# Kernel tuning notes

Measured on AMD Instinct MI355X. Metric: run time of the kernel, lower is better.

Reference implementation:

```python
import jax, jax.numpy as jnp
import numpy as np

D_MODEL = 1024
H = 16
D_K = D_MODEL // H
WINDOW = 256
NEG = -1.0e9


def setup_inputs() -> dict:
    key = jax.random.key(0)
    ks = jax.random.split(key, 12)
    B, S = 1, 4096
    scale = 1.0 / np.sqrt(D_MODEL)
    inp = {
        'q': jax.random.normal(ks[0], (B, S, D_MODEL), dtype=jnp.float32),
        'k': jax.random.normal(ks[1], (B, S, D_MODEL), dtype=jnp.float32),
        'v': jax.random.normal(ks[2], (B, S, D_MODEL), dtype=jnp.float32),
        'w_q': jax.random.normal(ks[3], (D_MODEL, D_MODEL), dtype=jnp.float32) * scale,
        'b_q': jnp.zeros((D_MODEL,), dtype=jnp.float32),
        'w_k': jax.random.normal(ks[4], (D_MODEL, D_MODEL), dtype=jnp.float32) * scale,
        'b_k': jnp.zeros((D_MODEL,), dtype=jnp.float32),
        'w_v': jax.random.normal(ks[5], (D_MODEL, D_MODEL), dtype=jnp.float32) * scale,
        'b_v': jnp.zeros((D_MODEL,), dtype=jnp.float32),
        'w_o': jax.random.normal(ks[6], (D_MODEL, D_MODEL), dtype=jnp.float32) * scale,
        'b_o': jnp.zeros((D_MODEL,), dtype=jnp.float32),
    }
    return inp


def _local_mask(seq_len: int, window_size: int) -> jnp.ndarray:
    left = (window_size - 1) // 2
    right = window_size - 1 - left
    row = jnp.arange(seq_len)[:, None]
    col = jnp.arange(seq_len)[None, :]
    return (col >= row - left) & (col <= row + right)  # [S, S] bool


def reference(q, k, v, w_q, b_q, w_k, b_k, w_v, b_v, w_o, b_o):
    B, Sq, _ = q.shape
    Sk = k.shape[1]
    # projections (torch Linear: x @ W.T + b) -> [B, h, S, d_k]
    query = (q @ w_q.T + b_q).reshape(B, Sq, H, D_K).transpose(0, 2, 1, 3)
    key = (k @ w_k.T + b_k).reshape(B, Sk, H, D_K).transpose(0, 2, 1, 3)
    value = (v @ w_v.T + b_v).reshape(B, Sk, H, D_K).transpose(0, 2, 1, 3)

    scores = jnp.einsum('bhqd,bhkd->bhqk', query, key) / jnp.sqrt(
        jnp.asarray(D_K, dtype=query.dtype))
    if Sq == Sk:
        mask = _local_mask(Sq, WINDOW)  # [S, S]
        scores = jnp.where(mask[None, None], scores, jnp.asarray(NEG, scores.dtype))
    attn = jax.nn.softmax(scores, axis=-1)
    x = jnp.einsum('bhqk,bhkd->bhqd', attn, value)
    x = x.transpose(0, 2, 1, 3).reshape(B, Sq, D_MODEL)
    return x @ w_o.T + b_o
```

## Files before the change

### kernel.cpp

```cpp
#include <hip/hip_runtime.h>

#define SEQ 4096
#define DM 1024
#define NH 16
#define DK 64

typedef _Float16 half8 __attribute__((ext_vector_type(8)));
typedef _Float16 half4v __attribute__((ext_vector_type(4)));
typedef float f32x4 __attribute__((ext_vector_type(4)));

#define MFMA16(a, b, c) __builtin_amdgcn_mfma_f32_16x16x32_f16((a), (b), (c), 0, 0, 0)
#define GLOAD_LDS(g, l)                                                                  \
    __builtin_amdgcn_global_load_lds((const __attribute__((address_space(1))) void*)(g), \
                                     (__attribute__((address_space(3))) void*)(l), 16, 0, 0)

__global__ void cvt_all(const float* __restrict__ q, const float* __restrict__ k,
                        const float* __restrict__ v, const float* __restrict__ wq,
                        const float* __restrict__ wk, const float* __restrict__ wv,
                        const float* __restrict__ wo, _Float16* __restrict__ qh,
                        _Float16* __restrict__ kh, _Float16* __restrict__ vh,
                        _Float16* __restrict__ wqh, _Float16* __restrict__ wkh,
                        _Float16* __restrict__ wvh, _Float16* __restrict__ woh) {
    int z = blockIdx.y;
    const float* src;
    _Float16* dst;
    int n;
    switch (z) {
    case 0: src = q;  dst = qh;  n = SEQ * DM; break;
    case 1: src = k;  dst = kh;  n = SEQ * DM; break;
    case 2: src = v;  dst = vh;  n = SEQ * DM; break;
    case 3: src = wq; dst = wqh; n = DM * DM;  break;
    case 4: src = wk; dst = wkh; n = DM * DM;  break;
    case 5: src = wv; dst = wvh; n = DM * DM;  break;
    default: src = wo; dst = woh; n = DM * DM; break;
    }
    int idx = (blockIdx.x * 256 + threadIdx.x) * 4;
    if (idx >= n) return;
    float4 f = *(const float4*)(src + idx);
    half4v h;
    h[0] = (_Float16)f.x; h[1] = (_Float16)f.y; h[2] = (_Float16)f.z; h[3] = (_Float16)f.w;
    *(half4v*)(dst + idx) = h;
}

template <int MT>
__device__ __forceinline__ void gemm_bk64(const _Float16* __restrict__ A,
                                          const _Float16* __restrict__ B, int m0, int n0,
                                          _Float16* As, _Float16* Bs, f32x4 (*acc)[4]) {
    constexpr int MI = MT / 32;
    constexpr int ACH = MT / 64;
    const int tid = threadIdx.x;
    const int wave = tid >> 6, lane = tid & 63;
    const int quad = lane >> 4, l16 = lane & 15;
    const int wr = (wave >> 1) * (MT / 2);
    const int wc = (wave & 1) * 64;
    const int srow = tid >> 2, scol = (tid & 3) * 8;

    for (int k0 = 0; k0 < DM; k0 += 64) {
#pragma unroll
        for (int p = 0; p < 2; ++p) {
            int kc = k0 + p * 32 + scol;
#pragma unroll
            for (int j = 0; j < ACH; ++j)
                GLOAD_LDS(A + (size_t)(m0 + j * 64 + srow) * DM + kc,
                          As + p * (MT * 32) + j * 2048 + tid * 8);
#pragma unroll
            for (int j = 0; j < 2; ++j)
                GLOAD_LDS(B + (size_t)(n0 + j * 64 + srow) * DM + kc,
                          Bs + p * 4096 + j * 2048 + tid * 8);
        }
        __syncthreads();
#pragma unroll
        for (int p = 0; p < 2; ++p) {
            half8 af[MI], bf[4];
#pragma unroll
            for (int mi = 0; mi < MI; ++mi)
                af[mi] = *(const half8*)&As[p * (MT * 32) + (wr + mi * 16 + l16) * 32 + quad * 8];
#pragma unroll
            for (int ni = 0; ni < 4; ++ni)
                bf[ni] = *(const half8*)&Bs[p * 4096 + (wc + ni * 16 + l16) * 32 + quad * 8];
#pragma unroll
            for (int mi = 0; mi < MI; ++mi)
#pragma unroll
                for (int ni = 0; ni < 4; ++ni)
                    acc[mi][ni] = MFMA16(af[mi], bf[ni], acc[mi][ni]);
        }
        __syncthreads();
    }
}

__global__ void __launch_bounds__(256, 3) gemm_qkv(
    const _Float16* __restrict__ qh, const _Float16* __restrict__ kh,
    const _Float16* __restrict__ vh, const _Float16* __restrict__ wqh,
    const _Float16* __restrict__ wkh, const _Float16* __restrict__ wvh,
    const float* __restrict__ bq, const float* __restrict__ bk, const float* __restrict__ bv,
    _Float16* __restrict__ Qo, _Float16* __restrict__ Ko, _Float16* __restrict__ Vt) {
    __shared__ _Float16 As[2 * 128 * 32];
    __shared__ _Float16 Bs[2 * 128 * 32];
    int z = blockIdx.z;
    const _Float16 *A, *B;
    const float* bias;
    float scale;
    if (z == 0) { A = qh; B = wqh; bias = bq; scale = 0.125f; }
    else if (z == 1) { A = kh; B = wkh; bias = bk; scale = 1.0f; }
    else { A = vh; B = wvh; bias = bv; scale = 1.0f; }

    int m0 = blockIdx.x * 128;
    int n0 = blockIdx.y * 128;
    f32x4 acc[4][4] = {};
    gemm_bk64<128>(A, B, m0, n0, As, Bs, acc);

    const int tid = threadIdx.x;
    const int wave = tid >> 6, lane = tid & 63;
    const int quad = lane >> 4, l16 = lane & 15;
    const int wr = (wave >> 1) * 64;
    const int wc = (wave & 1) * 64;
    float bs[4];
#pragma unroll
    for (int ni = 0; ni < 4; ++ni) bs[ni] = bias[n0 + wc + ni * 16 + l16];

    if (z < 2) {
        _Float16* C = (z == 0) ? Qo : Ko;
#pragma unroll
        for (int mi = 0; mi < 4; ++mi)
#pragma unroll
            for (int ni = 0; ni < 4; ++ni) {
                int m = m0 + wr + mi * 16 + quad * 4;
                int n = n0 + wc + ni * 16 + l16;
#pragma unroll
                for (int r = 0; r < 4; ++r)
                    C[(size_t)(m + r) * DM + n] = (_Float16)((acc[mi][ni][r] + bs[ni]) * scale);
            }
    } else {
#pragma unroll
        for (int mi = 0; mi < 4; ++mi)
#pragma unroll
            for (int ni = 0; ni < 4; ++ni) {
                int m = m0 + wr + mi * 16 + quad * 4;
                int n = n0 + wc + ni * 16 + l16;
                half4v p;
#pragma unroll
                for (int r = 0; r < 4; ++r) p[r] = (_Float16)(acc[mi][ni][r] + bs[ni]);
                *(half4v*)(Vt + (size_t)n * SEQ + m) = p;
            }
    }
}

__global__ void __launch_bounds__(256, 3) gemm_out(const _Float16* __restrict__ Xh,
                                                   const _Float16* __restrict__ woh,
                                                   const float* __restrict__ bo,
                                                   float* __restrict__ out) {
    __shared__ _Float16 As[2 * 64 * 32];
    __shared__ _Float16 Bs[2 * 128 * 32];
    int m0 = blockIdx.x * 64;
    int n0 = blockIdx.y * 128;
    f32x4 acc[2][4] = {};
    gemm_bk64<64>(Xh, woh, m0, n0, As, Bs, acc);

    const int tid = threadIdx.x;
    const int wave = tid >> 6, lane = tid & 63;
    const int quad = lane >> 4, l16 = lane & 15;
    const int wr = (wave >> 1) * 32;
    const int wc = (wave & 1) * 64;
#pragma unroll
    for (int mi = 0; mi < 2; ++mi)
#pragma unroll
        for (int ni = 0; ni < 4; ++ni) {
            int m = m0 + wr + mi * 16 + quad * 4;
            int n = n0 + wc + ni * 16 + l16;
            float b = bo[n];
#pragma unroll
            for (int r = 0; r < 4; ++r) out[(size_t)(m + r) * DM + n] = acc[mi][ni][r] + b;
        }
}

__global__ void attn_kernel(const _Float16* __restrict__ Q, const _Float16* __restrict__ K,
                            const _Float16* __restrict__ Vt, _Float16* __restrict__ X) {
    __shared__ _Float16 Pl[4][16][32];
    int tid = threadIdx.x;
    int wave = tid >> 6, lane = tid & 63;
    int quad = lane >> 4, l16 = lane & 15;
    int h = blockIdx.y;
    int bx = ((blockIdx.x & 7) << 3) + (blockIdx.x >> 3);
    int q0 = bx * 64 + wave * 16;

    const _Float16* Qp = Q + (size_t)(q0 + l16) * DM + h * DK + quad * 8;
    half8 aq0 = *(const half8*)(Qp);
    half8 aq1 = *(const half8*)(Qp + 32);

    float rowM[4], rowL[4];
    f32x4 o[4] = {};
#pragma unroll
    for (int r = 0; r < 4; ++r) { rowM[r] = -__builtin_inff(); rowL[r] = 0.f; }

    int kstart = (q0 > 127) ? ((q0 - 127) & ~31) : 0;
    int kend = q0 + 143;
    if (kend > SEQ - 1) kend = SEQ - 1;

    for (int kt = kstart; kt <= kend; kt += 32) {
        f32x4 s[2];
#pragma unroll
        for (int cf = 0; cf < 2; ++cf) {
            int krow = kt + cf * 16 + l16;
            const _Float16* Kp = K + (size_t)krow * DM + h * DK + quad * 8;
            half8 b0 = *(const half8*)(Kp);
            half8 b1 = *(const half8*)(Kp + 32);
            f32x4 z = {};
            z = MFMA16(aq0, b0, z);
            z = MFMA16(aq1, b1, z);
            s[cf] = z;
        }
        float mnew[4], alpha[4];
#pragma unroll
        for (int r = 0; r < 4; ++r) {
            int row = q0 + quad * 4 + r;
#pragma unroll
            for (int cf = 0; cf < 2; ++cf) {
                int key = kt + cf * 16 + l16;
                bool valid = (key >= row - 127) && (key <= row + 128);
                if (!valid) s[cf][r] = -1e30f;
            }
            float t = fmaxf(s[0][r], s[1][r]);
#pragma unroll
            for (int off = 1; off < 16; off <<= 1) t = fmaxf(t, __shfl_xor(t, off));
            mnew[r] = fmaxf(rowM[r], t);
            alpha[r] = __expf(rowM[r] - mnew[r]);
            float p0 = __expf(s[0][r] - mnew[r]);
            float p1 = __expf(s[1][r] - mnew[r]);
            Pl[wave][quad * 4 + r][l16] = (_Float16)p0;
            Pl[wave][quad * 4 + r][l16 + 16] = (_Float16)p1;
            float rs = p0 + p1;
#pragma unroll
            for (int off = 1; off < 16; off <<= 1) rs += __shfl_xor(rs, off);
            rowL[r] = rowL[r] * alpha[r] + rs;
            rowM[r] = mnew[r];
        }
#pragma unroll
        for (int ni = 0; ni < 4; ++ni)
#pragma unroll
            for (int r = 0; r < 4; ++r) o[ni][r] *= alpha[r];
        half8 ap = *(const half8*)&Pl[wave][l16][quad * 8];
#pragma unroll
        for (int ni = 0; ni < 4; ++ni) {
            const _Float16* Vp = Vt + (size_t)(h * DK + ni * 16 + l16) * SEQ + kt + quad * 8;
            half8 bv = *(const half8*)(Vp);
            o[ni] = MFMA16(ap, bv, o[ni]);
        }
    }

    float rinv[4];
#pragma unroll
    for (int r = 0; r < 4; ++r) rinv[r] = 1.0f / rowL[r];
#pragma unroll
    for (int ni = 0; ni < 4; ++ni) {
        int n = h * DK + ni * 16 + l16;
#pragma unroll
        for (int r = 0; r < 4; ++r) {
            int m = q0 + quad * 4 + r;
            X[(size_t)m * DM + n] = (_Float16)(o[ni][r] * rinv[r]);
        }
    }
}

extern "C" void kernel_launch(void* const* d_in, const int* in_sizes, int n_in, void* d_out,
                              int out_size, void* d_ws, size_t ws_size, hipStream_t stream) {
    const float* q  = (const float*)d_in[0];
    const float* k  = (const float*)d_in[1];
    const float* v  = (const float*)d_in[2];
    const float* wq = (const float*)d_in[3];
    const float* bq = (const float*)d_in[4];
    const float* wk = (const float*)d_in[5];
    const float* bk = (const float*)d_in[6];
    const float* wv = (const float*)d_in[7];
    const float* bv = (const float*)d_in[8];
    const float* wo = (const float*)d_in[9];
    const float* bo = (const float*)d_in[10];

    const size_t SZ_T = (size_t)SEQ * DM * sizeof(_Float16);
    const size_t SZ_W = (size_t)DM * DM * sizeof(_Float16);
    char* p = (char*)d_ws;
    _Float16* qh  = (_Float16*)(p);
    _Float16* kh  = (_Float16*)(p + SZ_T);
    _Float16* vh  = (_Float16*)(p + 2 * SZ_T);
    _Float16* wqh = (_Float16*)(p + 3 * SZ_T);
    _Float16* wkh = (_Float16*)(p + 3 * SZ_T + SZ_W);
    _Float16* wvh = (_Float16*)(p + 3 * SZ_T + 2 * SZ_W);
    _Float16* woh = (_Float16*)(p + 3 * SZ_T + 3 * SZ_W);
    _Float16* Qo  = (_Float16*)(p + 3 * SZ_T + 4 * SZ_W);
    _Float16* Ko  = (_Float16*)(p + 4 * SZ_T + 4 * SZ_W);
    _Float16* Vt  = (_Float16*)(p + 5 * SZ_T + 4 * SZ_W);
    _Float16* Xh  = qh;

    cvt_all<<<dim3(4096, 7), 256, 0, stream>>>(q, k, v, wq, wk, wv, wo, qh, kh, vh, wqh, wkh,
                                               wvh, woh);
    gemm_qkv<<<dim3(32, 8, 3), 256, 0, stream>>>(qh, kh, vh, wqh, wkh, wvh, bq, bk, bv, Qo, Ko,
                                                 Vt);
    attn_kernel<<<dim3(SEQ / 64, NH), 256, 0, stream>>>(Qo, Ko, Vt, Xh);
    gemm_out<<<dim3(64, 8), 256, 0, stream>>>(Xh, woh, bo, (float*)d_out);
}
```

Baseline: 213.6 us.

## Software-pipeline attention K loads, MFMA row sums, and widen conversion kernel

The attention loop becomes a fixed 10-tile fully unrolled loop with K fragments double-buffered in registers and V loads issued before the score MFMAs, so memory latency overlaps compute. The row-sum shuffle reduction is replaced by an MFMA of the probability tile against a ones vector, and launch bounds are added. The conversion kernel now processes 8 elements per thread with half the grid. Edge tiles are clamped and masked, which adds some redundant work for sequence-boundary blocks.

```diff
diff --git a/kernel.cpp b/kernel.cpp
--- a/kernel.cpp
+++ b/kernel.cpp
@@ -34,12 +34,14 @@
     case 5: src = wv; dst = wvh; n = DM * DM;  break;
     default: src = wo; dst = woh; n = DM * DM; break;
     }
-    int idx = (blockIdx.x * 256 + threadIdx.x) * 4;
+    int idx = (blockIdx.x * 256 + threadIdx.x) * 8;
     if (idx >= n) return;
-    float4 f = *(const float4*)(src + idx);
-    half4v h;
-    h[0] = (_Float16)f.x; h[1] = (_Float16)f.y; h[2] = (_Float16)f.z; h[3] = (_Float16)f.w;
-    *(half4v*)(dst + idx) = h;
+    float4 f0 = *(const float4*)(src + idx);
+    float4 f1 = *(const float4*)(src + idx + 4);
+    half8 h;
+    h[0] = (_Float16)f0.x; h[1] = (_Float16)f0.y; h[2] = (_Float16)f0.z; h[3] = (_Float16)f0.w;
+    h[4] = (_Float16)f1.x; h[5] = (_Float16)f1.y; h[6] = (_Float16)f1.z; h[7] = (_Float16)f1.w;
+    *(half8*)(dst + idx) = h;
 }
 
 template <int MT>
@@ -173,78 +175,95 @@
         }
 }
 
-__global__ void attn_kernel(const _Float16* __restrict__ Q, const _Float16* __restrict__ K,
-                            const _Float16* __restrict__ Vt, _Float16* __restrict__ X) {
+__global__ void __launch_bounds__(256, 4) attn_kernel(const _Float16* __restrict__ Q,
+                                                      const _Float16* __restrict__ K,
+                                                      const _Float16* __restrict__ Vt,
+                                                      _Float16* __restrict__ X) {
     __shared__ _Float16 Pl[4][16][32];
-    int tid = threadIdx.x;
-    int wave = tid >> 6, lane = tid & 63;
-    int quad = lane >> 4, l16 = lane & 15;
-    int h = blockIdx.y;
-    int bx = ((blockIdx.x & 7) << 3) + (blockIdx.x >> 3);
-    int q0 = bx * 64 + wave * 16;
+    const int tid = threadIdx.x;
+    const int wave = tid >> 6, lane = tid & 63;
+    const int quad = lane >> 4, l16 = lane & 15;
+    const int h = blockIdx.y;
+    const int bx = ((blockIdx.x & 7) << 3) + (blockIdx.x >> 3);
+    const int q0 = bx * 64 + wave * 16;
 
     const _Float16* Qp = Q + (size_t)(q0 + l16) * DM + h * DK + quad * 8;
-    half8 aq0 = *(const half8*)(Qp);
-    half8 aq1 = *(const half8*)(Qp + 32);
+    const half8 aq0 = *(const half8*)(Qp);
+    const half8 aq1 = *(const half8*)(Qp + 32);
+    const half8 ones = {(_Float16)1, (_Float16)1, (_Float16)1, (_Float16)1,
+                        (_Float16)1, (_Float16)1, (_Float16)1, (_Float16)1};
 
     float rowM[4], rowL[4];
     f32x4 o[4] = {};
 #pragma unroll
     for (int r = 0; r < 4; ++r) { rowM[r] = -__builtin_inff(); rowL[r] = 0.f; }
 
-    int kstart = (q0 > 127) ? ((q0 - 127) & ~31) : 0;
-    int kend = q0 + 143;
-    if (kend > SEQ - 1) kend = SEQ - 1;
-
-    for (int kt = kstart; kt <= kend; kt += 32) {
-        f32x4 s[2];
-#pragma unroll
-        for (int cf = 0; cf < 2; ++cf) {
-            int krow = kt + cf * 16 + l16;
-            const _Float16* Kp = K + (size_t)krow * DM + h * DK + quad * 8;
-            half8 b0 = *(const half8*)(Kp);
-            half8 b1 = *(const half8*)(Kp + 32);
-            f32x4 z = {};
-            z = MFMA16(aq0, b0, z);
-            z = MFMA16(aq1, b1, z);
-            s[cf] = z;
-        }
-        float mnew[4], alpha[4];
+    const int kstart = (q0 > 127) ? ((q0 - 127) & ~31) : 0;
+
+    auto loadK = [&](int kt, half8* kb) {
+        int kr0 = kt + l16;       kr0 = kr0 < SEQ ? kr0 : SEQ - 1;
+        int kr1 = kt + 16 + l16;  kr1 = kr1 < SEQ ? kr1 : SEQ - 1;
+        const _Float16* p0 = K + (size_t)kr0 * DM + h * DK + quad * 8;
+        const _Float16* p1 = K + (size_t)kr1 * DM + h * DK + quad * 8;
+        kb[0] = *(const half8*)p0;
+        kb[1] = *(const half8*)(p0 + 32);
+        kb[2] = *(const half8*)p1;
+        kb[3] = *(const half8*)(p1 + 32);
+    };
+
+    auto body = [&](int kt, const half8* kb) {
+        int vcol = kt + quad * 8;
+        int vc = vcol < SEQ ? vcol : 0;
+        half8 vv[4];
+#pragma unroll
+        for (int ni = 0; ni < 4; ++ni)
+            vv[ni] = *(const half8*)(Vt + (size_t)(h * DK + ni * 16 + l16) * SEQ + vc);
+
+        f32x4 s0 = {}, s1 = {};
+        s0 = MFMA16(aq0, kb[0], s0);
+        s0 = MFMA16(aq1, kb[1], s0);
+        s1 = MFMA16(aq0, kb[2], s1);
+        s1 = MFMA16(aq1, kb[3], s1);
+
+        const int key0 = kt + l16, key1 = kt + 16 + l16;
+        float alpha[4];
 #pragma unroll
         for (int r = 0; r < 4; ++r) {
             int row = q0 + quad * 4 + r;
-#pragma unroll
-            for (int cf = 0; cf < 2; ++cf) {
-                int key = kt + cf * 16 + l16;
-                bool valid = (key >= row - 127) && (key <= row + 128);
-                if (!valid) s[cf][r] = -1e30f;
-            }
-            float t = fmaxf(s[0][r], s[1][r]);
-#pragma unroll
-            for (int off = 1; off < 16; off <<= 1) t = fmaxf(t, __shfl_xor(t, off));
-            mnew[r] = fmaxf(rowM[r], t);
-            alpha[r] = __expf(rowM[r] - mnew[r]);
-            float p0 = __expf(s[0][r] - mnew[r]);
-            float p1 = __expf(s[1][r] - mnew[r]);
-            Pl[wave][quad * 4 + r][l16] = (_Float16)p0;
-            Pl[wave][quad * 4 + r][l16 + 16] = (_Float16)p1;
-            float rs = p0 + p1;
-#pragma unroll
-            for (int off = 1; off < 16; off <<= 1) rs += __shfl_xor(rs, off);
-            rowL[r] = rowL[r] * alpha[r] + rs;
-            rowM[r] = mnew[r];
-        }
-#pragma unroll
-        for (int ni = 0; ni < 4; ++ni)
+            float x0 = (key0 >= row - 127 && key0 <= row + 128 && key0 < SEQ) ? s0[r] : -1e30f;
+            float x1 = (key1 >= row - 127 && key1 <= row + 128 && key1 < SEQ) ? s1[r] : -1e30f;
+            float m = fmaxf(x0, x1);
+#pragma unroll
+            for (int off = 1; off < 16; off <<= 1) m = fmaxf(m, __shfl_xor(m, off));
+            float mnew = fmaxf(rowM[r], m);
+            alpha[r] = __expf(rowM[r] - mnew);
+            float p0f = __expf(x0 - mnew);
+            float p1f = __expf(x1 - mnew);
+            Pl[wave][quad * 4 + r][l16] = (_Float16)p0f;
+            Pl[wave][quad * 4 + r][l16 + 16] = (_Float16)p1f;
+            rowM[r] = mnew;
+        }
+        half8 ap = *(const half8*)&Pl[wave][l16][quad * 8];
+        f32x4 ts = {};
+        ts = MFMA16(ap, ones, ts);
+#pragma unroll
+        for (int r = 0; r < 4; ++r) rowL[r] = rowL[r] * alpha[r] + ts[r];
+#pragma unroll
+        for (int ni = 0; ni < 4; ++ni) {
 #pragma unroll
             for (int r = 0; r < 4; ++r) o[ni][r] *= alpha[r];
-        half8 ap = *(const half8*)&Pl[wave][l16][quad * 8];
-#pragma unroll
-        for (int ni = 0; ni < 4; ++ni) {
-            const _Float16* Vp = Vt + (size_t)(h * DK + ni * 16 + l16) * SEQ + kt + quad * 8;
-            half8 bv = *(const half8*)(Vp);
-            o[ni] = MFMA16(ap, bv, o[ni]);
-        }
+            o[ni] = MFMA16(ap, vv[ni], o[ni]);
+        }
+    };
+
+    half8 kbA[4], kbB[4];
+    loadK(kstart, kbA);
+#pragma unroll
+    for (int tt = 0; tt < 5; ++tt) {
+        loadK(kstart + (tt * 2 + 1) * 32, kbB);
+        body(kstart + tt * 2 * 32, kbA);
+        if (tt < 4) loadK(kstart + (tt * 2 + 2) * 32, kbA);
+        body(kstart + (tt * 2 + 1) * 32, kbB);
     }
 
     float rinv[4];
@@ -290,7 +309,7 @@
     _Float16* Vt  = (_Float16*)(p + 5 * SZ_T + 4 * SZ_W);
     _Float16* Xh  = qh;
 
-    cvt_all<<<dim3(4096, 7), 256, 0, stream>>>(q, k, v, wq, wk, wv, wo, qh, kh, vh, wqh, wkh,
+    cvt_all<<<dim3(2048, 7), 256, 0, stream>>>(q, k, v, wq, wk, wv, wo, qh, kh, vh, wqh, wkh,
                                                wvh, woh);
     gemm_qkv<<<dim3(32, 8, 3), 256, 0, stream>>>(qh, kh, vh, wqh, wkh, wvh, bq, bk, bv, Qo, Ko,
                                                  Vt);
```

New measurement: 220.2 us. 3.1% more time.

## Fuse all four stages into one persistent cooperative kernel with grid syncs

Applied to the files above, without the earlier changes.

Replaces the four separate launches (convert, QKV GEMM, attention, output GEMM) with a single persistent cooperative kernel of 512 blocks. The stages are separated by grid.sync() and each stage uses grid-stride or tile loops. The aim is to remove launch overhead and inter-kernel gaps. In exchange, occupancy is capped at 2 blocks per CU, the QKV GEMM runs 768 tiles over 512 blocks with an uneven tail, and each grid-wide barrier adds its own cost.

```diff
diff --git a/kernel.cpp b/kernel.cpp
--- a/kernel.cpp
+++ b/kernel.cpp
@@ -1,4 +1,7 @@
 #include <hip/hip_runtime.h>
+#include <hip/hip_cooperative_groups.h>
+
+namespace cg = cooperative_groups;
 
 #define SEQ 4096
 #define DM 1024
@@ -13,34 +16,6 @@
 #define GLOAD_LDS(g, l)                                                                  \
     __builtin_amdgcn_global_load_lds((const __attribute__((address_space(1))) void*)(g), \
                                      (__attribute__((address_space(3))) void*)(l), 16, 0, 0)
-
-__global__ void cvt_all(const float* __restrict__ q, const float* __restrict__ k,
-                        const float* __restrict__ v, const float* __restrict__ wq,
-                        const float* __restrict__ wk, const float* __restrict__ wv,
-                        const float* __restrict__ wo, _Float16* __restrict__ qh,
-                        _Float16* __restrict__ kh, _Float16* __restrict__ vh,
-                        _Float16* __restrict__ wqh, _Float16* __restrict__ wkh,
-                        _Float16* __restrict__ wvh, _Float16* __restrict__ woh) {
-    int z = blockIdx.y;
-    const float* src;
-    _Float16* dst;
-    int n;
-    switch (z) {
-    case 0: src = q;  dst = qh;  n = SEQ * DM; break;
-    case 1: src = k;  dst = kh;  n = SEQ * DM; break;
-    case 2: src = v;  dst = vh;  n = SEQ * DM; break;
-    case 3: src = wq; dst = wqh; n = DM * DM;  break;
-    case 4: src = wk; dst = wkh; n = DM * DM;  break;
-    case 5: src = wv; dst = wvh; n = DM * DM;  break;
-    default: src = wo; dst = woh; n = DM * DM; break;
-    }
-    int idx = (blockIdx.x * 256 + threadIdx.x) * 4;
-    if (idx >= n) return;
-    float4 f = *(const float4*)(src + idx);
-    half4v h;
-    h[0] = (_Float16)f.x; h[1] = (_Float16)f.y; h[2] = (_Float16)f.z; h[3] = (_Float16)f.w;
-    *(half4v*)(dst + idx) = h;
-}
 
 template <int MT>
 __device__ __forceinline__ void gemm_bk64(const _Float16* __restrict__ A,
@@ -88,176 +63,224 @@
     }
 }
 
-__global__ void __launch_bounds__(256, 3) gemm_qkv(
-    const _Float16* __restrict__ qh, const _Float16* __restrict__ kh,
-    const _Float16* __restrict__ vh, const _Float16* __restrict__ wqh,
-    const _Float16* __restrict__ wkh, const _Float16* __restrict__ wvh,
-    const float* __restrict__ bq, const float* __restrict__ bk, const float* __restrict__ bv,
-    _Float16* __restrict__ Qo, _Float16* __restrict__ Ko, _Float16* __restrict__ Vt) {
+__global__ void __launch_bounds__(256, 2) fused_mha(
+    const float* __restrict__ q, const float* __restrict__ k, const float* __restrict__ v,
+    const float* __restrict__ wq, const float* __restrict__ bq, const float* __restrict__ wk,
+    const float* __restrict__ bk, const float* __restrict__ wv, const float* __restrict__ bv,
+    const float* __restrict__ wo, const float* __restrict__ bo, char* __restrict__ ws,
+    float* __restrict__ out) {
     __shared__ _Float16 As[2 * 128 * 32];
     __shared__ _Float16 Bs[2 * 128 * 32];
-    int z = blockIdx.z;
-    const _Float16 *A, *B;
-    const float* bias;
-    float scale;
-    if (z == 0) { A = qh; B = wqh; bias = bq; scale = 0.125f; }
-    else if (z == 1) { A = kh; B = wkh; bias = bk; scale = 1.0f; }
-    else { A = vh; B = wvh; bias = bv; scale = 1.0f; }
-
-    int m0 = blockIdx.x * 128;
-    int n0 = blockIdx.y * 128;
-    f32x4 acc[4][4] = {};
-    gemm_bk64<128>(A, B, m0, n0, As, Bs, acc);
-
+
+    const size_t SZ_T = (size_t)SEQ * DM * sizeof(_Float16);
+    const size_t SZ_W = (size_t)DM * DM * sizeof(_Float16);
+    _Float16* qh  = (_Float16*)(ws);
+    _Float16* kh  = (_Float16*)(ws + SZ_T);
+    _Float16* vh  = (_Float16*)(ws + 2 * SZ_T);
+    _Float16* wqh = (_Float16*)(ws + 3 * SZ_T);
+    _Float16* wkh = (_Float16*)(ws + 3 * SZ_T + SZ_W);
+    _Float16* wvh = (_Float16*)(ws + 3 * SZ_T + 2 * SZ_W);
+    _Float16* woh = (_Float16*)(ws + 3 * SZ_T + 3 * SZ_W);
+    _Float16* Qo  = (_Float16*)(ws + 3 * SZ_T + 4 * SZ_W);
+    _Float16* Ko  = (_Float16*)(ws + 4 * SZ_T + 4 * SZ_W);
+    _Float16* Vt  = (_Float16*)(ws + 5 * SZ_T + 4 * SZ_W);
+    _Float16* Xh  = qh;
+
+    cg::grid_group grid = cg::this_grid();
     const int tid = threadIdx.x;
     const int wave = tid >> 6, lane = tid & 63;
     const int quad = lane >> 4, l16 = lane & 15;
-    const int wr = (wave >> 1) * 64;
-    const int wc = (wave & 1) * 64;
-    float bs[4];
-#pragma unroll
-    for (int ni = 0; ni < 4; ++ni) bs[ni] = bias[n0 + wc + ni * 16 + l16];
-
-    if (z < 2) {
-        _Float16* C = (z == 0) ? Qo : Ko;
-#pragma unroll
-        for (int mi = 0; mi < 4; ++mi)
+
+    {
+        const int gbase = (blockIdx.x * 256 + tid) * 8;
+        const int stride = 512 * 256 * 8;
+#pragma unroll 1
+        for (int z = 0; z < 7; ++z) {
+            const float* src;
+            _Float16* dst;
+            int n;
+            switch (z) {
+            case 0: src = q;  dst = qh;  n = SEQ * DM; break;
+            case 1: src = k;  dst = kh;  n = SEQ * DM; break;
+            case 2: src = v;  dst = vh;  n = SEQ * DM; break;
+            case 3: src = wq; dst = wqh; n = DM * DM;  break;
+            case 4: src = wk; dst = wkh; n = DM * DM;  break;
+            case 5: src = wv; dst = wvh; n = DM * DM;  break;
+            default: src = wo; dst = woh; n = DM * DM; break;
+            }
+#pragma unroll 1
+            for (int i = gbase; i < n; i += stride) {
+                float4 f0 = *(const float4*)(src + i);
+                float4 f1 = *(const float4*)(src + i + 4);
+                half8 h;
+                h[0] = (_Float16)f0.x; h[1] = (_Float16)f0.y;
+                h[2] = (_Float16)f0.z; h[3] = (_Float16)f0.w;
+                h[4] = (_Float16)f1.x; h[5] = (_Float16)f1.y;
+                h[6] = (_Float16)f1.z; h[7] = (_Float16)f1.w;
+                *(half8*)(dst + i) = h;
+            }
+        }
+    }
+    grid.sync();
+
+    {
+#pragma unroll 1
+        for (int t = blockIdx.x; t < 768; t += 512) {
+            const int z = t >> 8;
+            const int tt = t & 255;
+            const int m0 = (tt >> 3) * 128;
+            const int n0 = (tt & 7) * 128;
+            const _Float16* A = (z == 0) ? qh : (z == 1) ? kh : vh;
+            const _Float16* B = (z == 0) ? wqh : (z == 1) ? wkh : wvh;
+            const float* bias = (z == 0) ? bq : (z == 1) ? bk : bv;
+            const float scale = (z == 0) ? 0.125f : 1.0f;
+
+            f32x4 acc[4][4] = {};
+            gemm_bk64<128>(A, B, m0, n0, As, Bs, acc);
+
+            const int wr = (wave >> 1) * 64;
+            const int wc = (wave & 1) * 64;
+            float bs[4];
+#pragma unroll
+            for (int ni = 0; ni < 4; ++ni) bs[ni] = bias[n0 + wc + ni * 16 + l16];
+
+            if (z < 2) {
+                _Float16* C = (z == 0) ? Qo : Ko;
+#pragma unroll
+                for (int mi = 0; mi < 4; ++mi)
+#pragma unroll
+                    for (int ni = 0; ni < 4; ++ni) {
+                        int m = m0 + wr + mi * 16 + quad * 4;
+                        int n = n0 + wc + ni * 16 + l16;
+#pragma unroll
+                        for (int r = 0; r < 4; ++r)
+                            C[(size_t)(m + r) * DM + n] =
+                                (_Float16)((acc[mi][ni][r] + bs[ni]) * scale);
+                    }
+            } else {
+#pragma unroll
+                for (int mi = 0; mi < 4; ++mi)
+#pragma unroll
+                    for (int ni = 0; ni < 4; ++ni) {
+                        int m = m0 + wr + mi * 16 + quad * 4;
+                        int n = n0 + wc + ni * 16 + l16;
+                        half4v p;
+#pragma unroll
+                        for (int r = 0; r < 4; ++r) p[r] = (_Float16)(acc[mi][ni][r] + bs[ni]);
+                        *(half4v*)(Vt + (size_t)n * SEQ + m) = p;
+                    }
+            }
+        }
+    }
+    grid.sync();
+
+    {
+        _Float16(*Pl)[16][32] = (_Float16(*)[16][32])As;
+        const int gw = blockIdx.x * 4 + wave;
+#pragma unroll 1
+        for (int u = gw; u < 4096; u += 2048) {
+            const int h = u & 15;
+            const int q0 = (u >> 4) * 16;
+
+            const _Float16* Qp = Qo + (size_t)(q0 + l16) * DM + h * DK + quad * 8;
+            half8 aq0 = *(const half8*)(Qp);
+            half8 aq1 = *(const half8*)(Qp + 32);
+
+            float rowM[4], rowL[4];
+            f32x4 o[4] = {};
+#pragma unroll
+            for (int r = 0; r < 4; ++r) { rowM[r] = -__builtin_inff(); rowL[r] = 0.f; }
+
+            int kstart = (q0 > 127) ? ((q0 - 127) & ~31) : 0;
+            int kend = q0 + 143;
+            if (kend > SEQ - 1) kend = SEQ - 1;
+
+            for (int kt = kstart; kt <= kend; kt += 32) {
+                f32x4 s[2];
+#pragma unroll
+                for (int cf = 0; cf < 2; ++cf) {
+                    int krow = kt + cf * 16 + l16;
+                    const _Float16* Kp = Ko + (size_t)krow * DM + h * DK + quad * 8;
+                    half8 b0 = *(const half8*)(Kp);
+                    half8 b1 = *(const half8*)(Kp + 32);
+                    f32x4 zz = {};
+                    zz = MFMA16(aq0, b0, zz);
+                    zz = MFMA16(aq1, b1, zz);
+                    s[cf] = zz;
+                }
+                float mnew[4], alpha[4];
+#pragma unroll
+                for (int r = 0; r < 4; ++r) {
+                    int row = q0 + quad * 4 + r;
+#pragma unroll
+                    for (int cf = 0; cf < 2; ++cf) {
+                        int key = kt + cf * 16 + l16;
+                        bool valid = (key >= row - 127) && (key <= row + 128);
+                        if (!valid) s[cf][r] = -1e30f;
+                    }
+                    float t = fmaxf(s[0][r], s[1][r]);
+#pragma unroll
+                    for (int off = 1; off < 16; off <<= 1) t = fmaxf(t, __shfl_xor(t, off));
+                    mnew[r] = fmaxf(rowM[r], t);
+                    alpha[r] = __expf(rowM[r] - mnew[r]);
+                    float p0 = __expf(s[0][r] - mnew[r]);
+                    float p1 = __expf(s[1][r] - mnew[r]);
+                    Pl[wave][quad * 4 + r][l16] = (_Float16)p0;
+                    Pl[wave][quad * 4 + r][l16 + 16] = (_Float16)p1;
+                    float rs = p0 + p1;
+#pragma unroll
+                    for (int off = 1; off < 16; off <<= 1) rs += __shfl_xor(rs, off);
+                    rowL[r] = rowL[r] * alpha[r] + rs;
+                    rowM[r] = mnew[r];
+                }
+#pragma unroll
+                for (int ni = 0; ni < 4; ++ni)
+#pragma unroll
+                    for (int r = 0; r < 4; ++r) o[ni][r] *= alpha[r];
+                half8 ap = *(const half8*)&Pl[wave][l16][quad * 8];
+#pragma unroll
+                for (int ni = 0; ni < 4; ++ni) {
+                    const _Float16* Vp =
+                        Vt + (size_t)(h * DK + ni * 16 + l16) * SEQ + kt + quad * 8;
+                    half8 bv = *(const half8*)(Vp);
+                    o[ni] = MFMA16(ap, bv, o[ni]);
+                }
+            }
+
+            float rinv[4];
+#pragma unroll
+            for (int r = 0; r < 4; ++r) rinv[r] = 1.0f / rowL[r];
+#pragma unroll
+            for (int ni = 0; ni < 4; ++ni) {
+                int n = h * DK + ni * 16 + l16;
+#pragma unroll
+                for (int r = 0; r < 4; ++r) {
+                    int m = q0 + quad * 4 + r;
+                    Xh[(size_t)m * DM + n] = (_Float16)(o[ni][r] * rinv[r]);
+                }
+            }
+        }
+    }
+    grid.sync();
+
+    {
+        const int m0 = (blockIdx.x >> 3) * 64;
+        const int n0 = (blockIdx.x & 7) * 128;
+        f32x4 acc[2][4] = {};
+        gemm_bk64<64>(Xh, woh, m0, n0, As, Bs, acc);
+
+        const int wr = (wave >> 1) * 32;
+        const int wc = (wave & 1) * 64;
+#pragma unroll
+        for (int mi = 0; mi < 2; ++mi)
 #pragma unroll
             for (int ni = 0; ni < 4; ++ni) {
                 int m = m0 + wr + mi * 16 + quad * 4;
                 int n = n0 + wc + ni * 16 + l16;
-#pragma unroll
-                for (int r = 0; r < 4; ++r)
-                    C[(size_t)(m + r) * DM + n] = (_Float16)((acc[mi][ni][r] + bs[ni]) * scale);
-            }
-    } else {
-#pragma unroll
-        for (int mi = 0; mi < 4; ++mi)
-#pragma unroll
-            for (int ni = 0; ni < 4; ++ni) {
-                int m = m0 + wr + mi * 16 + quad * 4;
-                int n = n0 + wc + ni * 16 + l16;
-                half4v p;
-#pragma unroll
-                for (int r = 0; r < 4; ++r) p[r] = (_Float16)(acc[mi][ni][r] + bs[ni]);
-                *(half4v*)(Vt + (size_t)n * SEQ + m) = p;
-            }
-    }
-}
-
-__global__ void __launch_bounds__(256, 3) gemm_out(const _Float16* __restrict__ Xh,
-                                                   const _Float16* __restrict__ woh,
-                                                   const float* __restrict__ bo,
-                                                   float* __restrict__ out) {
-    __shared__ _Float16 As[2 * 64 * 32];
-    __shared__ _Float16 Bs[2 * 128 * 32];
-    int m0 = blockIdx.x * 64;
-    int n0 = blockIdx.y * 128;
-    f32x4 acc[2][4] = {};
-    gemm_bk64<64>(Xh, woh, m0, n0, As, Bs, acc);
-
-    const int tid = threadIdx.x;
-    const int wave = tid >> 6, lane = tid & 63;
-    const int quad = lane >> 4, l16 = lane & 15;
-    const int wr = (wave >> 1) * 32;
-    const int wc = (wave & 1) * 64;
-#pragma unroll
-    for (int mi = 0; mi < 2; ++mi)
-#pragma unroll
-        for (int ni = 0; ni < 4; ++ni) {
-            int m = m0 + wr + mi * 16 + quad * 4;
-            int n = n0 + wc + ni * 16 + l16;
-            float b = bo[n];
-#pragma unroll
-            for (int r = 0; r < 4; ++r) out[(size_t)(m + r) * DM + n] = acc[mi][ni][r] + b;
-        }
-}
-
-__global__ void attn_kernel(const _Float16* __restrict__ Q, const _Float16* __restrict__ K,
-                            const _Float16* __restrict__ Vt, _Float16* __restrict__ X) {
-    __shared__ _Float16 Pl[4][16][32];
-    int tid = threadIdx.x;
-    int wave = tid >> 6, lane = tid & 63;
-    int quad = lane >> 4, l16 = lane & 15;
-    int h = blockIdx.y;
-    int bx = ((blockIdx.x & 7) << 3) + (blockIdx.x >> 3);
-    int q0 = bx * 64 + wave * 16;
-
-    const _Float16* Qp = Q + (size_t)(q0 + l16) * DM + h * DK + quad * 8;
-    half8 aq0 = *(const half8*)(Qp);
-    half8 aq1 = *(const half8*)(Qp + 32);
-
-    float rowM[4], rowL[4];
-    f32x4 o[4] = {};
-#pragma unroll
-    for (int r = 0; r < 4; ++r) { rowM[r] = -__builtin_inff(); rowL[r] = 0.f; }
-
-    int kstart = (q0 > 127) ? ((q0 - 127) & ~31) : 0;
-    int kend = q0 + 143;
-    if (kend > SEQ - 1) kend = SEQ - 1;
-
-    for (int kt = kstart; kt <= kend; kt += 32) {
-        f32x4 s[2];
-#pragma unroll
-        for (int cf = 0; cf < 2; ++cf) {
-            int krow = kt + cf * 16 + l16;
-            const _Float16* Kp = K + (size_t)krow * DM + h * DK + quad * 8;
-            half8 b0 = *(const half8*)(Kp);
-            half8 b1 = *(const half8*)(Kp + 32);
-            f32x4 z = {};
-            z = MFMA16(aq0, b0, z);
-            z = MFMA16(aq1, b1, z);
-            s[cf] = z;
-        }
-        float mnew[4], alpha[4];
-#pragma unroll
-        for (int r = 0; r < 4; ++r) {
-            int row = q0 + quad * 4 + r;
-#pragma unroll
-            for (int cf = 0; cf < 2; ++cf) {
-                int key = kt + cf * 16 + l16;
-                bool valid = (key >= row - 127) && (key <= row + 128);
-                if (!valid) s[cf][r] = -1e30f;
-            }
-            float t = fmaxf(s[0][r], s[1][r]);
-#pragma unroll
-            for (int off = 1; off < 16; off <<= 1) t = fmaxf(t, __shfl_xor(t, off));
-            mnew[r] = fmaxf(rowM[r], t);
-            alpha[r] = __expf(rowM[r] - mnew[r]);
-            float p0 = __expf(s[0][r] - mnew[r]);
-            float p1 = __expf(s[1][r] - mnew[r]);
-            Pl[wave][quad * 4 + r][l16] = (_Float16)p0;
-            Pl[wave][quad * 4 + r][l16 + 16] = (_Float16)p1;
-            float rs = p0 + p1;
-#pragma unroll
-            for (int off = 1; off < 16; off <<= 1) rs += __shfl_xor(rs, off);
-            rowL[r] = rowL[r] * alpha[r] + rs;
-            rowM[r] = mnew[r];
-        }
-#pragma unroll
-        for (int ni = 0; ni < 4; ++ni)
-#pragma unroll
-            for (int r = 0; r < 4; ++r) o[ni][r] *= alpha[r];
-        half8 ap = *(const half8*)&Pl[wave][l16][quad * 8];
-#pragma unroll
-        for (int ni = 0; ni < 4; ++ni) {
-            const _Float16* Vp = Vt + (size_t)(h * DK + ni * 16 + l16) * SEQ + kt + quad * 8;
-            half8 bv = *(const half8*)(Vp);
-            o[ni] = MFMA16(ap, bv, o[ni]);
-        }
-    }
-
-    float rinv[4];
-#pragma unroll
-    for (int r = 0; r < 4; ++r) rinv[r] = 1.0f / rowL[r];
-#pragma unroll
-    for (int ni = 0; ni < 4; ++ni) {
-        int n = h * DK + ni * 16 + l16;
-#pragma unroll
-        for (int r = 0; r < 4; ++r) {
-            int m = q0 + quad * 4 + r;
-            X[(size_t)m * DM + n] = (_Float16)(o[ni][r] * rinv[r]);
-        }
+                float b = bo[n];
+#pragma unroll
+                for (int r = 0; r < 4; ++r) out[(size_t)(m + r) * DM + n] = acc[mi][ni][r] + b;
+            }
     }
 }
 
@@ -274,26 +297,9 @@
     const float* bv = (const float*)d_in[8];
     const float* wo = (const float*)d_in[9];
     const float* bo = (const float*)d_in[10];
-
-    const size_t SZ_T = (size_t)SEQ * DM * sizeof(_Float16);
-    const size_t SZ_W = (size_t)DM * DM * sizeof(_Float16);
-    char* p = (char*)d_ws;
-    _Float16* qh  = (_Float16*)(p);
-    _Float16* kh  = (_Float16*)(p + SZ_T);
-    _Float16* vh  = (_Float16*)(p + 2 * SZ_T);
-    _Float16* wqh = (_Float16*)(p + 3 * SZ_T);
-    _Float16* wkh = (_Float16*)(p + 3 * SZ_T + SZ_W);
-    _Float16* wvh = (_Float16*)(p + 3 * SZ_T + 2 * SZ_W);
-    _Float16* woh = (_Float16*)(p + 3 * SZ_T + 3 * SZ_W);
-    _Float16* Qo  = (_Float16*)(p + 3 * SZ_T + 4 * SZ_W);
-    _Float16* Ko  = (_Float16*)(p + 4 * SZ_T + 4 * SZ_W);
-    _Float16* Vt  = (_Float16*)(p + 5 * SZ_T + 4 * SZ_W);
-    _Float16* Xh  = qh;
-
-    cvt_all<<<dim3(4096, 7), 256, 0, stream>>>(q, k, v, wq, wk, wv, wo, qh, kh, vh, wqh, wkh,
-                                               wvh, woh);
-    gemm_qkv<<<dim3(32, 8, 3), 256, 0, stream>>>(qh, kh, vh, wqh, wkh, wvh, bq, bk, bv, Qo, Ko,
-                                                 Vt);
-    attn_kernel<<<dim3(SEQ / 64, NH), 256, 0, stream>>>(Qo, Ko, Vt, Xh);
-    gemm_out<<<dim3(64, 8), 256, 0, stream>>>(Xh, woh, bo, (float*)d_out);
+    char* ws = (char*)d_ws;
+    float* out = (float*)d_out;
+
+    void* args[] = {&q, &k, &v, &wq, &bq, &wk, &bk, &wv, &bv, &wo, &bo, &ws, &out};
+    hipLaunchCooperativeKernel((const void*)fused_mha, dim3(512), dim3(256), args, 0, stream);
 }
```

Result: slower. 426.7 us (+99.8%).
